# Performance work log

Measured on AMD Instinct MI355X. Metric: run time of the kernel, lower is better.

Reference implementation:

```python
import jax, jax.numpy as jnp
import numpy as np

N, CIN, T, V, P, K, NCLS = 8, 3, 300, 25, 3, 9, 60
EPS = 1e-5


def setup_inputs() -> dict:
    key = jax.random.key(0)
    ks = jax.random.split(key, 10)
    rn = lambda k, s: jax.random.normal(k, s, jnp.float32) * 0.05
    return {
        "x": jax.random.normal(ks[0], (N, CIN, T, V), jnp.float32),
        "A": jax.random.uniform(ks[1], (P, V, V), jnp.float32),
        "bn_in_g": jnp.ones((V * CIN,), jnp.float32),
        "bn_in_b": jnp.zeros((V * CIN,), jnp.float32),
        "fin_W": rn(ks[2], (64, CIN)), "fin_b": jnp.zeros((64,), jnp.float32),
        "imp0": jnp.ones((V, V), jnp.float32), "imp1": jnp.ones((V, V), jnp.float32),
        "imp2": jnp.ones((V, V), jnp.float32), "imp3": jnp.ones((V, V), jnp.float32),
        "W0": rn(ks[3], (64 * P, 64)), "g0": jnp.ones((64,), jnp.float32), "b0": jnp.zeros((64,), jnp.float32),
        "W1": rn(ks[4], (128 * P, 64)), "g1": jnp.ones((128,), jnp.float32), "b1": jnp.zeros((128,), jnp.float32),
        "Wr1": rn(ks[5], (128, 64)), "gr1": jnp.ones((128,), jnp.float32), "br1": jnp.zeros((128,), jnp.float32),
        "W2": rn(ks[6], (256 * P, 128)), "g2": jnp.ones((256,), jnp.float32), "b2": jnp.zeros((256,), jnp.float32),
        "Wr2": rn(ks[7], (256, 128)), "gr2": jnp.ones((256,), jnp.float32), "br2": jnp.zeros((256,), jnp.float32),
        "W3": rn(ks[8], (256 * P, 256)), "g3": jnp.ones((256,), jnp.float32), "b3": jnp.zeros((256,), jnp.float32),
        "fout_W": rn(ks[9], (NCLS, 256)), "fout_b": jnp.zeros((NCLS,), jnp.float32),
    }


def _bn(x, g, b, axes):
    # training-mode batchnorm (batch statistics), matching nn.BatchNorm in train()
    m = jnp.mean(x, axes, keepdims=True)
    v = jnp.var(x, axes, keepdims=True)
    return (x - m) * jax.lax.rsqrt(v + EPS) * g + b


def _lt_matrix(t):
    # lower-triangular-style shift matrix: lt[r, c] = 1 iff 0 <= c - r < K (stride 1)
    d = jnp.arange(t)[None, :] - jnp.arange(t)[:, None]
    return ((d >= 0) & (d < K)).astype(jnp.float32)


def _layer(x, A, W, g, b, lt, res, final_relu):
    # x: (N, Cin, T, V); W: (P*Cout, Cin); A: (P, V, V); lt: (T, T)
    n, _, t, v = x.shape
    cout = W.shape[0] // P
    y = jnp.einsum('nctv,kc->nktv', x, W).reshape(n, P, cout, t, v)   # 1x1 conv + split/stack
    z = jnp.einsum('npctv,pvw->npctw', y, A)                          # spatial graph matmul
    u = jnp.einsum('npctv,ts->npcsv', z, lt)                          # dense LxL temporal matmul
    h = u.sum(1)                                                      # sum over partitions -> (N, Cout, T, V)
    h = jax.nn.relu(_bn(h, g[None, :, None, None], b[None, :, None, None], (0, 2, 3)))
    out = h + res
    return jax.nn.relu(out) if final_relu else out


def reference(x, A, bn_in_g, bn_in_b, fin_W, fin_b, imp0, imp1, imp2, imp3,
              W0, g0, b0, W1, g1, b1, Wr1, gr1, br1,
              W2, g2, b2, Wr2, gr2, br2, W3, g3, b3, fout_W, fout_b):
    n, c, t, v = x.shape
    # input BatchNorm1d over (V*C) channels
    xp = x.transpose(0, 3, 1, 2).reshape(n, v * c, t)
    xp = _bn(xp, bn_in_g[None, :, None], bn_in_b[None, :, None], (0, 2))
    h = xp.reshape(n, v, c, t).transpose(0, 2, 3, 1)                  # (N, C, T, V)
    h = jnp.einsum('nctv,oc->notv', h, fin_W) + fin_b[None, :, None, None]
    lt = _lt_matrix(t)
    # layer 0: no residual, no final relu (Dropout only, p=0 -> identity)
    h = _layer(h, A * imp0, W0, g0, b0, lt, 0.0, False)
    # layer 1: 64 -> 128, conv+BN residual
    r1 = _bn(jnp.einsum('nctv,oc->notv', h, Wr1), gr1[None, :, None, None], br1[None, :, None, None], (0, 2, 3))
    h = _layer(h, A * imp1, W1, g1, b1, lt, r1, True)
    # layer 2: 128 -> 256, conv+BN residual
    r2 = _bn(jnp.einsum('nctv,oc->notv', h, Wr2), gr2[None, :, None, None], br2[None, :, None, None], (0, 2, 3))
    h = _layer(h, A * imp2, W2, g2, b2, lt, r2, True)
    # layer 3: 256 -> 256, identity residual
    h = _layer(h, A * imp3, W3, g3, b3, lt, h, True)
    # average pool over joints, 1x1 classification conv
    h = h.mean(-1, keepdims=True)                                     # (N, 256, T, 1)
    out = jnp.einsum('nctv,oc->notv', h, fout_W) + fout_b[None, :, None, None]
    return out[..., 0]                                                # (N, num_classes, T)
```

## Files before the change

### kernel.cpp

```cpp
#include <hip/hip_runtime.h>

#define EPS 1e-5f
typedef unsigned short u16;
typedef __attribute__((ext_vector_type(8))) short short8;
typedef __attribute__((ext_vector_type(4))) float f32x4;

__device__ __forceinline__ float bf2f(u16 u) {
  union { unsigned int i; float f; } c; c.i = ((unsigned int)u) << 16; return c.f;
}
__device__ __forceinline__ u16 f2bf(float f) {
  union { float f; unsigned int i; } c; c.f = f;
  unsigned int u = c.i;
  u += 0x7fffu + ((u >> 16) & 1u);
  return (u16)(u >> 16);
}
__device__ __forceinline__ unsigned int cvt_pk_bf16(float lo, float hi) {
  unsigned int r;
  asm("v_cvt_pk_bf16_f32 %0, %1, %2" : "=v"(r) : "v"(lo), "v"(hi));
  return r;
}
__device__ __forceinline__ short8 load8u(const u16* p) {
  short8 v; __builtin_memcpy(&v, p, 16); return v;
}
__device__ __forceinline__ void gload16(const u16* g, u16* l) {
  __builtin_amdgcn_global_load_lds(
      (__attribute__((address_space(1))) void*)(void*)g,
      (__attribute__((address_space(3))) void*)l, 16, 0, 0);
}

__device__ __forceinline__ void prep_w_elem(const float* W, u16* Wt,
    int cin, int cout, int P, int idx) {
  const int K = P*cin;
  const int co = idx / K, k = idx % K;
  const int p = k / cin, ci = k % cin;
  Wt[idx] = f2bf(W[((size_t)(p*cout + co))*cin + ci]);
}

__global__ __launch_bounds__(256) void k_prep_all(
    const float* __restrict__ A,
    const float* __restrict__ i0, const float* __restrict__ i1,
    const float* __restrict__ i2, const float* __restrict__ i3,
    const float* __restrict__ W0, const float* __restrict__ W1,
    const float* __restrict__ Wr1, const float* __restrict__ W2,
    const float* __restrict__ Wr2, const float* __restrict__ W3,
    u16* W0t, u16* W1t, u16* Wr1t, u16* W2t,
    u16* Wr2t, u16* W3t, u16* ATb, u16* hpad) {
  int idx = blockIdx.x*256 + threadIdx.x;
  if (idx < 12288) { prep_w_elem(W0,  W0t,  64,  64,  3, idx); return; }
  idx -= 12288;
  if (idx < 24576) { prep_w_elem(W1,  W1t,  64,  128, 3, idx); return; }
  idx -= 24576;
  if (idx < 8192)  { prep_w_elem(Wr1, Wr1t, 64,  128, 1, idx); return; }
  idx -= 8192;
  if (idx < 98304) { prep_w_elem(W2,  W2t,  128, 256, 3, idx); return; }
  idx -= 98304;
  if (idx < 32768) { prep_w_elem(Wr2, Wr2t, 128, 256, 1, idx); return; }
  idx -= 32768;
  if (idx < 196608){ prep_w_elem(W3,  W3t,  256, 256, 3, idx); return; }
  idx -= 196608;
  if (idx < 12288) {
    const int l = idx / 3072, r = idx % 3072;
    const int p = r / 1024, wv = r % 1024;
    const int w = wv >> 5, v = wv & 31;
    float val = 0.f;
    if (w < 25 && v < 25) {
      const float* imp = (l==0)?i0:(l==1)?i1:(l==2)?i2:i3;
      val = A[(p*25 + v)*25 + w] * imp[v*25 + w];
    }
    ATb[idx] = f2bf(val);
    return;
  }
  idx -= 12288;
  if (idx < 32) hpad[idx] = 0;
}

__global__ __launch_bounds__(256) void k_bn_in_stats(const float* __restrict__ x,
    const float* __restrict__ g, const float* __restrict__ b,
    float* __restrict__ iscale, float* __restrict__ ishift) {
  const int j = blockIdx.x;
  const int c = j % 3, v = j / 3;
  const int tid = threadIdx.x;
  float s = 0.f, q = 0.f;
  for (int i = tid; i < 2400; i += 256) {
    const int n = i / 300, t = i % 300;
    const float val = x[(((size_t)n*3 + c)*300 + t)*25 + v];
    s += val; q += val*val;
  }
  __shared__ float rs[256], rq[256];
  rs[tid] = s; rq[tid] = q;
  __syncthreads();
  for (int off = 128; off > 0; off >>= 1) {
    if (tid < off) { rs[tid] += rs[tid+off]; rq[tid] += rq[tid+off]; }
    __syncthreads();
  }
  if (tid == 0) {
    const float mean = rs[0] / 2400.f;
    const float var  = rq[0] / 2400.f - mean*mean;
    const float sc = g[j] * rsqrtf(var + EPS);
    iscale[j] = sc;
    ishift[j] = b[j] - mean*sc;
  }
}

__global__ __launch_bounds__(256) void k_fin(const float* __restrict__ x,
    const float* __restrict__ iscale, const float* __restrict__ ishift,
    const float* __restrict__ fW, const float* __restrict__ fb,
    u16* __restrict__ H) {
  const int n = blockIdx.y;
  const int t0 = blockIdx.x * 10;
  const int tid = threadIdx.x;
  __shared__ float xn[3][250];
  __shared__ float wsh[64][3];
  __shared__ float bsh[64];
  if (tid < 192) wsh[tid/3][tid%3] = fW[tid];
  if (tid < 64)  bsh[tid] = fb[tid];
  for (int i = tid; i < 750; i += 256) {
    const int c = i / 250, pos = i % 250;
    const int t = t0 + pos/25, v = pos%25;
    const int j = v*3 + c;
    xn[c][pos] = x[(((size_t)n*3 + c)*300 + t)*25 + v] * iscale[j] + ishift[j];
  }
  __syncthreads();
  for (int e = tid; e < 64*250; e += 256) {
    const int o = e / 250, pos = e % 250;
    float acc = bsh[o]
              + xn[0][pos]*wsh[o][0] + xn[1][pos]*wsh[o][1] + xn[2][pos]*wsh[o][2];
    const int t = t0 + pos/25, v = pos%25;
    H[(((size_t)n*64 + o)*300 + t)*25 + v] = f2bf(acc);
  }
}

__global__ __launch_bounds__(256) void k_hmk(const u16* __restrict__ H,
    u16* __restrict__ Hmk, int cin) {
  const int m0  = blockIdx.x * 64;
  const int ci0 = blockIdx.y * 32;
  const int n   = blockIdx.z;
  __shared__ u16 tile[32][72];
  const int tid = threadIdx.x;
  {
    const int ci = tid >> 3, chunk = tid & 7;
    const int m = m0 + chunk * 8;
    const u16* src = &H[(size_t)(n*cin + ci0 + ci)*7500];
    short8 v;
    if (m + 7 < 7500) {
      v = load8u(&src[m]);
    } else {
      #pragma unroll
      for (int j = 0; j < 8; ++j)
        ((u16*)&v)[j] = (m + j < 7500) ? src[m + j] : (u16)0;
    }
    *(short8*)&tile[ci][chunk*8] = v;
  }
  __syncthreads();
  const int mr = tid >> 2, cq = (tid & 3) * 8;
  const int m = m0 + mr;
  if (m < 7500) {
    short8 v;
    #pragma unroll
    for (int j = 0; j < 8; ++j) ((u16*)&v)[j] = tile[cq + j][mr];
    *(short8*)&Hmk[((size_t)n*7500 + m)*cin + ci0 + cq] = v;
  }
}

template<int CIN>
__global__ __launch_bounds__(256) void k_xa_mfma5(const u16* __restrict__ H,
    const u16* __restrict__ ATl, u16* __restrict__ XA) {
  constexpr int K = 3 * CIN;
  constexpr int ldz = K + 8;
  constexpr int ncit = CIN >> 4;
  constexpr int rowchunks = K >> 3;
  const int t0 = blockIdx.x * 2, n = blockIdx.y;
  const int tid = threadIdx.x, lane = tid & 63, wid = tid >> 6;
  const int lrow = lane & 15, lchunk = lane >> 4;
  extern __shared__ u16 zt[];

  short8 bf[3][2];
  #pragma unroll
  for (int p = 0; p < 3; ++p)
    #pragma unroll
    for (int wt = 0; wt < 2; ++wt)
      bf[p][wt] = *(const short8*)&ATl[(p*32 + wt*16 + lrow)*32 + lchunk*8];

  const int w0 = lrow;
  const int ciq = lchunk * 4;

  #pragma unroll
  for (int tl = 0; tl < 2; ++tl) {
    const int t = t0 + tl;
    if (tl) __syncthreads();
    for (int citile = wid; citile < ncit; citile += 4) {
      const int ci = citile*16 + lrow;
      const short8 af = load8u(&H[((size_t)(n*CIN + ci)*300 + t)*25 + lchunk*8]);
      #pragma unroll
      for (int p = 0; p < 3; ++p) {
        #pragma unroll
        for (int wt = 0; wt < 2; ++wt) {
          f32x4 acc = (f32x4){0.f, 0.f, 0.f, 0.f};
          acc = __builtin_amdgcn_mfma_f32_16x16x32_bf16(af, bf[p][wt], acc, 0, 0, 0);
          const int w = wt*16 + w0;
          if (w < 25) {
            uint2 pk;
            pk.x = cvt_pk_bf16(acc[0], acc[1]);
            pk.y = cvt_pk_bf16(acc[2], acc[3]);
            *(uint2*)&zt[w*ldz + p*CIN + citile*16 + ciq] = pk;
          }
        }
      }
    }
    __syncthreads();
    const size_t mbase = ((size_t)n*300 + t)*25;
    for (int i = tid; i < 25*rowchunks; i += 256) {
      const int row = i / rowchunks, c = i % rowchunks;
      *(short8*)&XA[(mbase + row)*K + c*8] = *(const short8*)&zt[row*ldz + c*8];
    }
  }
}

template<int COUT>
__global__ __launch_bounds__(512) void k_gemmT(const u16* __restrict__ Asrc,
    const u16* __restrict__ Bsrc, u16* __restrict__ Cb, int K) {
  constexpr int NI = COUT / 64;
  const int m0 = blockIdx.x * 128;
  const int tid = threadIdx.x;
  const int lane = tid & 63, wid = tid >> 6;
  const int wm = (wid >> 2) * 64, wn = (wid & 3) * (COUT / 4);

  __shared__ u16 As[128*64];
  __shared__ u16 Bs[COUT*64];

  f32x4 acc[4][NI];
  #pragma unroll
  for (int mi = 0; mi < 4; ++mi)
    #pragma unroll
    for (int ni = 0; ni < NI; ++ni) acc[mi][ni] = (f32x4){0.f,0.f,0.f,0.f};

  const int rA = tid >> 3, cA = tid & 7;

  const int nkt = K >> 6;
  for (int kt = 0; kt < nkt; ++kt) {
    const int kbase = kt * 64;
    __syncthreads();
    #pragma unroll
    for (int i = 0; i < 2; ++i) {
      const int idx = tid + i*512;
      const int r = rA + i*64;
      int m = m0 + r; if (m > 59999) m = 59999;
      gload16(Asrc + (size_t)m*K + kbase + ((cA ^ (r & 7)) * 8), &As[idx*8]);
    }
    #pragma unroll
    for (int i = 0; i < NI; ++i) {
      const int idx = tid + i*512;
      const int r = rA + i*64;
      gload16(Bsrc + (size_t)r*K + kbase + ((cA ^ (r & 7)) * 8), &Bs[idx*8]);
    }
    __syncthreads();
    #pragma unroll
    for (int kc = 0; kc < 2; ++kc) {
      const int kchunk = kc*4 + (lane >> 4);
      short8 a[4], b[NI];
      #pragma unroll
      for (int mi = 0; mi < 4; ++mi) {
        const int m = wm + mi*16 + (lane & 15);
        a[mi] = *(const short8*)&As[m*64 + ((kchunk ^ (m & 7)) * 8)];
      }
      #pragma unroll
      for (int ni = 0; ni < NI; ++ni) {
        const int r = wn + ni*16 + (lane & 15);
        b[ni] = *(const short8*)&Bs[r*64 + ((kchunk ^ (r & 7)) * 8)];
      }
      #pragma unroll
      for (int mi = 0; mi < 4; ++mi)
        #pragma unroll
        for (int ni = 0; ni < NI; ++ni)
          acc[mi][ni] = __builtin_amdgcn_mfma_f32_16x16x32_bf16(a[mi], b[ni], acc[mi][ni], 0, 0, 0);
    }
  }

  const int mrow = (lane >> 4) * 4;
  #pragma unroll
  for (int mi = 0; mi < 4; ++mi) {
    const int mb = m0 + wm + mi*16 + mrow;
    if (mb >= 60000) continue;
    #pragma unroll
    for (int ni = 0; ni < NI; ++ni) {
      const int co = wn + ni*16 + (lane & 15);
      uint2 pk;
      pk.x = cvt_pk_bf16(acc[mi][ni][0], acc[mi][ni][1]);
      pk.y = cvt_pk_bf16(acc[mi][ni][2], acc[mi][ni][3]);
      *(uint2*)&Cb[(size_t)co*60000 + mb] = pk;
    }
  }
}

__global__ __launch_bounds__(256) void k_bn_part_win(const u16* __restrict__ G,
    float* __restrict__ part, int cout) {
  const int c = blockIdx.x, n = blockIdx.y;
  const int tid = threadIdx.x;
  const u16* gb = G + (size_t)c*60000 + (size_t)n*7500;
  float s = 0.f, q = 0.f;
  for (int i = tid; i < 7500; i += 256) {
    const int ss = i / 25, w = i % 25;
    float S = 0.f;
    if (ss >= 8) {
      #pragma unroll
      for (int d = 0; d < 9; ++d) S += bf2f(gb[i - d*25]);
    } else {
      for (int tt = 0; tt <= ss; ++tt) S += bf2f(gb[tt*25 + w]);
    }
    s += S; q += S*S;
  }
  __shared__ float rs[256], rq[256];
  rs[tid] = s; rq[tid] = q;
  __syncthreads();
  for (int off = 128; off > 0; off >>= 1) {
    if (tid < off) { rs[tid] += rs[tid+off]; rq[tid] += rq[tid+off]; }
    __syncthreads();
  }
  if (tid == 0) {
    part[((size_t)c*8 + n)*2]     = rs[0];
    part[((size_t)c*8 + n)*2 + 1] = rq[0];
  }
}

__global__ __launch_bounds__(256) void k_bn_part_plain(const u16* __restrict__ R,
    float* __restrict__ part, int cout) {
  const int c = blockIdx.x, n = blockIdx.y;
  const int tid = threadIdx.x;
  const u16* rb = R + (size_t)c*60000 + (size_t)n*7500;
  float s = 0.f, q = 0.f;
  for (int i = tid; i < 7500; i += 256) {
    const float val = bf2f(rb[i]);
    s += val; q += val*val;
  }
  __shared__ float rs[256], rq[256];
  rs[tid] = s; rq[tid] = q;
  __syncthreads();
  for (int off = 128; off > 0; off >>= 1) {
    if (tid < off) { rs[tid] += rs[tid+off]; rq[tid] += rq[tid+off]; }
    __syncthreads();
  }
  if (tid == 0) {
    part[((size_t)c*8 + n)*2]     = rs[0];
    part[((size_t)c*8 + n)*2 + 1] = rq[0];
  }
}

__global__ __launch_bounds__(256) void k_apply2(const u16* __restrict__ G,
    const u16* __restrict__ Rb, const u16* Hres,
    const float* __restrict__ part, const float* __restrict__ g, const float* __restrict__ b,
    const float* __restrict__ rpart, const float* __restrict__ rg, const float* __restrict__ rbb,
    u16* Out, float* HPout, int cout, int mode) {
  const int bc = blockIdx.x;
  const int c = bc % cout, n = bc / cout;
  __shared__ u16 os[7500];
  float s = 0.f, q = 0.f;
  #pragma unroll
  for (int i = 0; i < 8; ++i) {
    s += part[((size_t)c*8 + i)*2];
    q += part[((size_t)c*8 + i)*2 + 1];
  }
  const float mean = s / 60000.f;
  const float var  = q / 60000.f - mean*mean;
  const float sc = g[c] * rsqrtf(var + EPS);
  const float sh = b[c] - mean*sc;
  float rsc = 0.f, rsh = 0.f;
  if (mode == 1) {
    float s2 = 0.f, q2 = 0.f;
    #pragma unroll
    for (int i = 0; i < 8; ++i) {
      s2 += rpart[((size_t)c*8 + i)*2];
      q2 += rpart[((size_t)c*8 + i)*2 + 1];
    }
    const float m2 = s2 / 60000.f;
    const float v2 = q2 / 60000.f - m2*m2;
    rsc = rg[c] * rsqrtf(v2 + EPS);
    rsh = rbb[c] - m2*rsc;
  }
  const u16* gb = G + (size_t)c*60000 + (size_t)n*7500;
  const size_t rbase = (size_t)c*60000 + (size_t)n*7500;
  for (int i = threadIdx.x; i < 7500; i += 256) {
    const int ss = i / 25, w = i % 25;
    float S = 0.f;
    if (ss >= 8) {
      #pragma unroll
      for (int d = 0; d < 9; ++d) S += bf2f(gb[i - d*25]);
    } else {
      for (int tt = 0; tt <= ss; ++tt) S += bf2f(gb[tt*25 + w]);
    }
    const float h = fmaxf(S*sc + sh, 0.f);
    float o;
    if (mode == 0)      o = h;
    else if (mode == 1) o = fmaxf(h + (bf2f(Rb[rbase + i])*rsc + rsh), 0.f);
    else                o = fmaxf(h + bf2f(Hres[(size_t)bc*7500 + i]), 0.f);
    const u16 ob = f2bf(o);
    Out[(size_t)bc*7500 + i] = ob;
    if (HPout) os[i] = ob;
  }
  if (HPout) {
    __syncthreads();
    for (int t = threadIdx.x; t < 300; t += 256) {
      float ps = 0.f;
      #pragma unroll
      for (int v = 0; v < 25; ++v) ps += bf2f(os[t*25 + v]);
      HPout[(size_t)bc*300 + t] = ps * 0.04f;
    }
  }
}

__global__ __launch_bounds__(256) void k_fout3(const float* __restrict__ HP,
    const float* __restrict__ fW, const float* __restrict__ fb,
    float* __restrict__ out) {
  const int t = blockIdx.x, n = blockIdx.y;
  const int tid = threadIdx.x;
  __shared__ float hp[256];
  hp[tid] = HP[((size_t)n*256 + tid)*300 + t];
  __syncthreads();
  const int o = tid >> 2, kq = tid & 3;
  float s = 0.f;
  if (o < 60) {
    const float* wrow = fW + o*256 + kq*64;
    const float* hrow = hp + kq*64;
    #pragma unroll
    for (int c = 0; c < 64; c += 4) {
      const f32x4 w4 = *(const f32x4*)&wrow[c];
      const f32x4 h4 = *(const f32x4*)&hrow[c];
      s += w4[0]*h4[0] + w4[1]*h4[1] + w4[2]*h4[2] + w4[3]*h4[3];
    }
  }
  s += __shfl_xor(s, 1);
  s += __shfl_xor(s, 2);
  if (o < 60 && kq == 0)
    out[((size_t)n*60 + o)*300 + t] = s + fb[o];
}

extern "C" void kernel_launch(void* const* d_in, const int* in_sizes, int n_in,
                              void* d_out, int out_size, void* d_ws, size_t ws_size,
                              hipStream_t stream) {
  (void)in_sizes; (void)n_in; (void)out_size; (void)ws_size;
  const float* x     = (const float*)d_in[0];
  const float* A     = (const float*)d_in[1];
  const float* bng   = (const float*)d_in[2];
  const float* bnb   = (const float*)d_in[3];
  const float* finW  = (const float*)d_in[4];
  const float* finb  = (const float*)d_in[5];
  const float* imp0  = (const float*)d_in[6];
  const float* imp1  = (const float*)d_in[7];
  const float* imp2  = (const float*)d_in[8];
  const float* imp3  = (const float*)d_in[9];
  const float* W0    = (const float*)d_in[10];
  const float* g0    = (const float*)d_in[11];
  const float* b0    = (const float*)d_in[12];
  const float* W1    = (const float*)d_in[13];
  const float* g1    = (const float*)d_in[14];
  const float* b1    = (const float*)d_in[15];
  const float* Wr1   = (const float*)d_in[16];
  const float* gr1   = (const float*)d_in[17];
  const float* br1   = (const float*)d_in[18];
  const float* W2    = (const float*)d_in[19];
  const float* g2    = (const float*)d_in[20];
  const float* b2    = (const float*)d_in[21];
  const float* Wr2   = (const float*)d_in[22];
  const float* gr2   = (const float*)d_in[23];
  const float* br2   = (const float*)d_in[24];
  const float* W3    = (const float*)d_in[25];
  const float* g3    = (const float*)d_in[26];
  const float* b3    = (const float*)d_in[27];
  const float* foutW = (const float*)d_in[28];
  const float* foutb = (const float*)d_in[29];
  float* out = (float*)d_out;

  char* base = (char*)d_ws;
  u16*   Z    = (u16*)base;
  u16*   Hmk  = (u16*)base;
  float* HP   = (float*)(base + 40000000);
  float* PART = (float*)(base + 45000000);
  float* RPART= (float*)(base + 45100000);
  u16*   XA   = (u16*)(base + 61440000);
  u16*   Rb   = (u16*)(base + 107520000);
  u16*   Hct  = (u16*)(base + 153600000);
  u16*   HPAD = (u16*)(base + 184320000);
  u16*   ATb  = (u16*)(base + 185000000);
  u16*   WT   = (u16*)(base + 186777600);
  float* ST   = (float*)(base + 188000000);
  float* ISC = ST, *ISH = ST + 80;

  u16* W0t  = WT;
  u16* W1t  = WT + 12288;
  u16* Wr1t = WT + 36864;
  u16* W2t  = WT + 45056;
  u16* Wr2t = WT + 143360;
  u16* W3t  = WT + 176128;

  k_prep_all<<<1505, 256, 0, stream>>>(A, imp0, imp1, imp2, imp3,
      W0, W1, Wr1, W2, Wr2, W3, W0t, W1t, Wr1t, W2t, Wr2t, W3t, ATb, HPAD);

  k_bn_in_stats<<<75, 256, 0, stream>>>(x, bng, bnb, ISC, ISH);
  k_fin<<<dim3(30, 8), 256, 0, stream>>>(x, ISC, ISH, finW, finb, Hct);

  const int MT = 469;
  const int ldsK192 = 25 * (192 + 8) * 2;
  const int ldsK384 = 25 * (384 + 8) * 2;
  const int ldsK768 = 25 * (768 + 8) * 2;

  k_xa_mfma5<64><<<dim3(150, 8), 256, ldsK192, stream>>>(Hct, ATb, XA);
  k_gemmT<64><<<MT, 512, 0, stream>>>(XA, W0t, Z, 192);
  k_bn_part_win<<<dim3(64, 8), 256, 0, stream>>>(Z, PART, 64);
  k_apply2<<<8*64, 256, 0, stream>>>(Z, nullptr, nullptr, PART, g0, b0,
      nullptr, nullptr, nullptr, Hct, nullptr, 64, 0);

  k_hmk<<<dim3(118, 2, 8), 256, 0, stream>>>(Hct, Hmk, 64);
  k_xa_mfma5<64><<<dim3(150, 8), 256, ldsK192, stream>>>(Hct, ATb + 1*3072, XA);
  k_gemmT<128><<<MT, 512, 0, stream>>>(Hmk, Wr1t, Rb, 64);
  k_bn_part_plain<<<dim3(128, 8), 256, 0, stream>>>(Rb, RPART, 128);
  k_gemmT<128><<<MT, 512, 0, stream>>>(XA, W1t, Z, 192);
  k_bn_part_win<<<dim3(128, 8), 256, 0, stream>>>(Z, PART, 128);
  k_apply2<<<8*128, 256, 0, stream>>>(Z, Rb, nullptr, PART, g1, b1,
      RPART, gr1, br1, Hct, nullptr, 128, 1);

  k_hmk<<<dim3(118, 4, 8), 256, 0, stream>>>(Hct, Hmk, 128);
  k_xa_mfma5<128><<<dim3(150, 8), 256, ldsK384, stream>>>(Hct, ATb + 2*3072, XA);
  k_gemmT<256><<<MT, 512, 0, stream>>>(Hmk, Wr2t, Rb, 128);
  k_bn_part_plain<<<dim3(256, 8), 256, 0, stream>>>(Rb, RPART, 256);
  k_gemmT<256><<<MT, 512, 0, stream>>>(XA, W2t, Z, 384);
  k_bn_part_win<<<dim3(256, 8), 256, 0, stream>>>(Z, PART, 256);
  k_apply2<<<8*256, 256, 0, stream>>>(Z, Rb, nullptr, PART, g2, b2,
      RPART, gr2, br2, Hct, nullptr, 256, 1);

  k_xa_mfma5<256><<<dim3(150, 8), 256, ldsK768, stream>>>(Hct, ATb + 3*3072, XA);
  k_gemmT<256><<<MT, 512, 0, stream>>>(XA, W3t, Z, 768);
  k_bn_part_win<<<dim3(256, 8), 256, 0, stream>>>(Z, PART, 256);
  k_apply2<<<8*256, 256, 0, stream>>>(Z, nullptr, Hct, PART, g3, b3,
      nullptr, nullptr, nullptr, Hct, HP, 256, 2);

  k_fout3<<<dim3(300, 8), 256, 0, stream>>>(HP, foutW, foutb, out);
}
```

Baseline: 418.9 us.

## Fuse graph aggregation with channel GEMM into one per-timestep kernel

Replaces the separate XA aggregation kernel and the following k_gemmT with a single kernel, k_fz. Each block aggregates one timestep into LDS (padded to 32 rows), then multiplies it by the weight matrix with MFMA and writes Z directly. This removes the global write and re-read of the large XA intermediate and one launch per layer. In exchange, each block reads the full weight matrix straight from global/L2 memory with little reuse, since only 25 rows are useful. The Z stores are narrow 2-byte writes strided by channel, so memory traffic patterns could get worse for the wide layers.

```diff
diff --git a/kernel.cpp b/kernel.cpp
--- a/kernel.cpp
+++ b/kernel.cpp
@@ -162,14 +162,15 @@
   }
 }
 
-template<int CIN>
-__global__ __launch_bounds__(256) void k_xa_mfma5(const u16* __restrict__ H,
-    const u16* __restrict__ ATl, u16* __restrict__ XA) {
+template<int CIN, int COUT>
+__global__ __launch_bounds__(256) void k_fz(const u16* __restrict__ H,
+    const u16* __restrict__ ATl, const u16* __restrict__ Wt,
+    u16* __restrict__ Cb) {
   constexpr int K = 3 * CIN;
   constexpr int ldz = K + 8;
   constexpr int ncit = CIN >> 4;
-  constexpr int rowchunks = K >> 3;
-  const int t0 = blockIdx.x * 2, n = blockIdx.y;
+  constexpr int NCT = COUT / 64;
+  const int t = blockIdx.x, n = blockIdx.y;
   const int tid = threadIdx.x, lane = tid & 63, wid = tid >> 6;
   const int lrow = lane & 15, lchunk = lane >> 4;
   extern __shared__ u16 zt[];
@@ -181,37 +182,58 @@
     for (int wt = 0; wt < 2; ++wt)
       bf[p][wt] = *(const short8*)&ATl[(p*32 + wt*16 + lrow)*32 + lchunk*8];
 
-  const int w0 = lrow;
   const int ciq = lchunk * 4;
-
-  #pragma unroll
-  for (int tl = 0; tl < 2; ++tl) {
-    const int t = t0 + tl;
-    if (tl) __syncthreads();
-    for (int citile = wid; citile < ncit; citile += 4) {
-      const int ci = citile*16 + lrow;
-      const short8 af = load8u(&H[((size_t)(n*CIN + ci)*300 + t)*25 + lchunk*8]);
-      #pragma unroll
-      for (int p = 0; p < 3; ++p) {
-        #pragma unroll
-        for (int wt = 0; wt < 2; ++wt) {
-          f32x4 acc = (f32x4){0.f, 0.f, 0.f, 0.f};
-          acc = __builtin_amdgcn_mfma_f32_16x16x32_bf16(af, bf[p][wt], acc, 0, 0, 0);
-          const int w = wt*16 + w0;
-          if (w < 25) {
-            uint2 pk;
-            pk.x = cvt_pk_bf16(acc[0], acc[1]);
-            pk.y = cvt_pk_bf16(acc[2], acc[3]);
-            *(uint2*)&zt[w*ldz + p*CIN + citile*16 + ciq] = pk;
-          }
+  for (int citile = wid; citile < ncit; citile += 4) {
+    const int ci = citile*16 + lrow;
+    const short8 af = load8u(&H[((size_t)(n*CIN + ci)*300 + t)*25 + lchunk*8]);
+    #pragma unroll
+    for (int p = 0; p < 3; ++p) {
+      #pragma unroll
+      for (int wt = 0; wt < 2; ++wt) {
+        f32x4 z = (f32x4){0.f, 0.f, 0.f, 0.f};
+        z = __builtin_amdgcn_mfma_f32_16x16x32_bf16(af, bf[p][wt], z, 0, 0, 0);
+        const int w = wt*16 + lrow;
+        if (w < 25) {
+          uint2 pk;
+          pk.x = cvt_pk_bf16(z[0], z[1]);
+          pk.y = cvt_pk_bf16(z[2], z[3]);
+          *(uint2*)&zt[w*ldz + p*CIN + citile*16 + ciq] = pk;
         }
       }
     }
-    __syncthreads();
-    const size_t mbase = ((size_t)n*300 + t)*25;
-    for (int i = tid; i < 25*rowchunks; i += 256) {
-      const int row = i / rowchunks, c = i % rowchunks;
-      *(short8*)&XA[(mbase + row)*K + c*8] = *(const short8*)&zt[row*ldz + c*8];
+  }
+  __syncthreads();
+
+  const int co0 = (COUT/4) * wid;
+  f32x4 acc[2][NCT];
+  #pragma unroll
+  for (int mt = 0; mt < 2; ++mt)
+    #pragma unroll
+    for (int ct = 0; ct < NCT; ++ct) acc[mt][ct] = (f32x4){0.f,0.f,0.f,0.f};
+
+  for (int ks = 0; ks < K/32; ++ks) {
+    const short8 a0 = *(const short8*)&zt[(size_t)lrow*ldz      + ks*32 + lchunk*8];
+    const short8 a1 = *(const short8*)&zt[(size_t)(16+lrow)*ldz + ks*32 + lchunk*8];
+    #pragma unroll
+    for (int ct = 0; ct < NCT; ++ct) {
+      const int co = co0 + ct*16 + lrow;
+      const short8 b = *(const short8*)&Wt[(size_t)co*K + ks*32 + lchunk*8];
+      acc[0][ct] = __builtin_amdgcn_mfma_f32_16x16x32_bf16(a0, b, acc[0][ct], 0, 0, 0);
+      acc[1][ct] = __builtin_amdgcn_mfma_f32_16x16x32_bf16(a1, b, acc[1][ct], 0, 0, 0);
+    }
+  }
+
+  const size_t mbase = ((size_t)n*300 + t)*25;
+  #pragma unroll
+  for (int mt = 0; mt < 2; ++mt) {
+    const int m0 = mt*16 + lchunk*4;
+    #pragma unroll
+    for (int ct = 0; ct < NCT; ++ct) {
+      const int co = co0 + ct*16 + lrow;
+      #pragma unroll
+      for (int r = 0; r < 4; ++r)
+        if (m0 + r < 25)
+          Cb[(size_t)co*60000 + mbase + m0 + r] = f2bf(acc[mt][ct][r]);
     }
   }
 }
@@ -475,7 +497,6 @@
   float* HP   = (float*)(base + 40000000);
   float* PART = (float*)(base + 45000000);
   float* RPART= (float*)(base + 45100000);
-  u16*   XA   = (u16*)(base + 61440000);
   u16*   Rb   = (u16*)(base + 107520000);
   u16*   Hct  = (u16*)(base + 153600000);
   u16*   HPAD = (u16*)(base + 184320000);
@@ -498,36 +519,32 @@
   k_fin<<<dim3(30, 8), 256, 0, stream>>>(x, ISC, ISH, finW, finb, Hct);
 
   const int MT = 469;
-  const int ldsK192 = 25 * (192 + 8) * 2;
-  const int ldsK384 = 25 * (384 + 8) * 2;
-  const int ldsK768 = 25 * (768 + 8) * 2;
-
-  k_xa_mfma5<64><<<dim3(150, 8), 256, ldsK192, stream>>>(Hct, ATb, XA);
-  k_gemmT<64><<<MT, 512, 0, stream>>>(XA, W0t, Z, 192);
+  const int ldsK192 = 32 * (192 + 8) * 2;
+  const int ldsK384 = 32 * (384 + 8) * 2;
+  const int ldsK768 = 32 * (768 + 8) * 2;
+
+  k_fz<64,64><<<dim3(300, 8), 256, ldsK192, stream>>>(Hct, ATb, W0t, Z);
   k_bn_part_win<<<dim3(64, 8), 256, 0, stream>>>(Z, PART, 64);
   k_apply2<<<8*64, 256, 0, stream>>>(Z, nullptr, nullptr, PART, g0, b0,
       nullptr, nullptr, nullptr, Hct, nullptr, 64, 0);
 
   k_hmk<<<dim3(118, 2, 8), 256, 0, stream>>>(Hct, Hmk, 64);
-  k_xa_mfma5<64><<<dim3(150, 8), 256, ldsK192, stream>>>(Hct, ATb + 1*3072, XA);
   k_gemmT<128><<<MT, 512, 0, stream>>>(Hmk, Wr1t, Rb, 64);
   k_bn_part_plain<<<dim3(128, 8), 256, 0, stream>>>(Rb, RPART, 128);
-  k_gemmT<128><<<MT, 512, 0, stream>>>(XA, W1t, Z, 192);
+  k_fz<64,128><<<dim3(300, 8), 256, ldsK192, stream>>>(Hct, ATb + 1*3072, W1t, Z);
   k_bn_part_win<<<dim3(128, 8), 256, 0, stream>>>(Z, PART, 128);
   k_apply2<<<8*128, 256, 0, stream>>>(Z, Rb, nullptr, PART, g1, b1,
       RPART, gr1, br1, Hct, nullptr, 128, 1);
 
   k_hmk<<<dim3(118, 4, 8), 256, 0, stream>>>(Hct, Hmk, 128);
-  k_xa_mfma5<128><<<dim3(150, 8), 256, ldsK384, stream>>>(Hct, ATb + 2*3072, XA);
   k_gemmT<256><<<MT, 512, 0, stream>>>(Hmk, Wr2t, Rb, 128);
   k_bn_part_plain<<<dim3(256, 8), 256, 0, stream>>>(Rb, RPART, 256);
-  k_gemmT<256><<<MT, 512, 0, stream>>>(XA, W2t, Z, 384);
+  k_fz<128,256><<<dim3(300, 8), 256, ldsK384, stream>>>(Hct, ATb + 2*3072, W2t, Z);
   k_bn_part_win<<<dim3(256, 8), 256, 0, stream>>>(Z, PART, 256);
   k_apply2<<<8*256, 256, 0, stream>>>(Z, Rb, nullptr, PART, g2, b2,
       RPART, gr2, br2, Hct, nullptr, 256, 1);
 
-  k_xa_mfma5<256><<<dim3(150, 8), 256, ldsK768, stream>>>(Hct, ATb + 3*3072, XA);
-  k_gemmT<256><<<MT, 512, 0, stream>>>(XA, W3t, Z, 768);
+  k_fz<256,256><<<dim3(300, 8), 256, ldsK768, stream>>>(Hct, ATb + 3*3072, W3t, Z);
   k_bn_part_win<<<dim3(256, 8), 256, 0, stream>>>(Z, PART, 256);
   k_apply2<<<8*256, 256, 0, stream>>>(Z, nullptr, Hct, PART, g3, b3,
       nullptr, nullptr, nullptr, Hct, HP, 256, 2);
```

After: 559.5 us. 33.6% more time.
